# Performance work log

Measured on AMD Instinct MI355X. Metric: run time of the kernel, lower is better.

Reference implementation:

```python
import jax, jax.numpy as jnp
import numpy as np

TOP_K = 2

def setup_inputs() -> dict:
    key = jax.random.key(0)
    k1, k2 = jax.random.split(key)
    x = jax.random.normal(k1, (4, 4096, 4096), dtype=jnp.float32)
    # nn.Linear(hidden, experts, bias=False) weight: [num_experts, hidden]
    gate_w = jax.random.normal(k2, (64, 4096), dtype=jnp.float32) * (1.0 / np.sqrt(4096.0))
    return {"x": x, "gate_w": gate_w}

def reference(x, gate_w):
    # logits: [b, s, e] = x @ gate_w.T
    logits = jnp.einsum('bsh,eh->bse', x, gate_w)
    top_k_logits, top_k_indices = jax.lax.top_k(logits, TOP_K)  # [b, s, k]
    # softmax over top-k logits in float32, cast back to logits dtype
    probs = jax.nn.softmax(top_k_logits.astype(jnp.float32), axis=-1).astype(logits.dtype)
    return (logits, top_k_indices, probs)
```

## Files before the change

### kernel.cpp

```cpp
#include <hip/hip_runtime.h>
#include <math.h>

#define H 4096
#define E 64
#define BMROWS 16
#define NT 256
#define KQ 1024
#define BK 32
#define NWIN (KQ / BK)

typedef short bf16x8 __attribute__((ext_vector_type(8)));
typedef float f32x4  __attribute__((ext_vector_type(4)));

__device__ __forceinline__ unsigned f2bf_rne_u(float f) {
    unsigned u = __float_as_uint(f);
    return (u + 0x7fffu + ((u >> 16) & 1u)) >> 16;
}

__global__ __launch_bounds__(256) void convert_w(const float* __restrict__ w,
                                                 unsigned short* __restrict__ wh,
                                                 unsigned short* __restrict__ wl) {
    const int i = (blockIdx.x * 256 + threadIdx.x) * 4;
    float4 v = *(const float4*)(w + i);
    float vv[4] = {v.x, v.y, v.z, v.w};
    unsigned hh[4], ll[4];
#pragma unroll
    for (int j = 0; j < 4; ++j) {
        hh[j] = f2bf_rne_u(vv[j]);
        float r = vv[j] - __uint_as_float(hh[j] << 16);
        ll[j] = __float_as_uint(r) >> 16;
    }
    ushort4 h, l;
    h.x = (unsigned short)hh[0]; h.y = (unsigned short)hh[1];
    h.z = (unsigned short)hh[2]; h.w = (unsigned short)hh[3];
    l.x = (unsigned short)ll[0]; l.y = (unsigned short)ll[1];
    l.z = (unsigned short)ll[2]; l.w = (unsigned short)ll[3];
    *(ushort4*)(wh + i) = h;
    *(ushort4*)(wl + i) = l;
}

__device__ __forceinline__ void cvt8(const float4 a, const float4 b,
                                     bf16x8& hi, bf16x8& lo) {
    float v[8] = {a.x, a.y, a.z, a.w, b.x, b.y, b.z, b.w};
#pragma unroll
    for (int i = 0; i < 8; ++i) {
        const unsigned u = __float_as_uint(v[i]);
        const unsigned t = u + 0x7fffu + ((u >> 16) & 1u);
        const float    r = v[i] - __uint_as_float(t & 0xffff0000u);
        hi[i] = (short)(t >> 16);
        lo[i] = (short)(__float_as_uint(r) >> 16);
    }
}

__global__ __launch_bounds__(NT, 4) void router_kernel(
    const float* __restrict__ x,
    const unsigned short* __restrict__ wh,
    const unsigned short* __restrict__ wl,
    float* __restrict__ out, int M)
{
    __shared__ __align__(16) f32x4 merge[4][4][64];

    const int t    = threadIdx.x;
    const int lane = t & 63;
    const int wk   = t >> 6;
    const int m0   = blockIdx.x * BMROWS;
    const int col  = lane & 15;
    const int quad = lane >> 4;

    const int kbase = wk * KQ + quad * 8;

    const float* xp = x + (size_t)(m0 + col) * H + kbase;
    const unsigned short* whp = wh + (size_t)col * H + kbase;
    const unsigned short* wlp = wl + (size_t)col * H + kbase;

    f32x4 acc[4];
#pragma unroll
    for (int nt = 0; nt < 4; ++nt)
        acc[nt] = (f32x4){0.0f, 0.0f, 0.0f, 0.0f};

    float4 x0[2], x1[2], x2[2], x3[2];
    uint4  wr[8];

    auto loadx_into = [&](int win, float4 (&xb)[2]) {
        const int k = win * BK;
        xb[0] = *(const float4*)(xp + k);
        xb[1] = *(const float4*)(xp + k + 4);
    };
    auto loadw = [&](int win) {
        const int k = win * BK;
#pragma unroll
        for (int nt = 0; nt < 4; ++nt) {
            wr[nt]     = *(const uint4*)(whp + (size_t)(nt * 16) * H + k);
            wr[nt + 4] = *(const uint4*)(wlp + (size_t)(nt * 16) * H + k);
        }
    };

    auto step = [&](int win, float4 (&xc)[2], float4 (&xpref)[2]) {
        loadw(win);
        if (win + 3 < NWIN) loadx_into(win + 3, xpref);
        bf16x8 ah, al;
        cvt8(xc[0], xc[1], ah, al);
#pragma unroll
        for (int nt = 0; nt < 4; ++nt) {
            const bf16x8 bh = __builtin_bit_cast(bf16x8, wr[nt]);
            const bf16x8 bl = __builtin_bit_cast(bf16x8, wr[nt + 4]);
            acc[nt] = __builtin_amdgcn_mfma_f32_16x16x32_bf16(ah, bh, acc[nt], 0, 0, 0);
            acc[nt] = __builtin_amdgcn_mfma_f32_16x16x32_bf16(ah, bl, acc[nt], 0, 0, 0);
            acc[nt] = __builtin_amdgcn_mfma_f32_16x16x32_bf16(al, bh, acc[nt], 0, 0, 0);
        }
    };

    loadx_into(0, x0);
    loadx_into(1, x1);
    loadx_into(2, x2);

#pragma unroll 1
    for (int win = 0; win < NWIN; win += 4) {
        step(win,     x0, x3);
        step(win + 1, x1, x0);
        step(win + 2, x2, x1);
        step(win + 3, x3, x2);
    }

#pragma unroll
    for (int nt = 0; nt < 4; ++nt)
        merge[nt][wk][lane] = acc[nt];
    __syncthreads();

    if (wk != 0) return;

    f32x4 a2[4];
#pragma unroll
    for (int nt = 0; nt < 4; ++nt) {
        f32x4 s = acc[nt];
#pragma unroll
        for (int w = 1; w < 4; ++w)
            s += merge[nt][w][lane];
        a2[nt] = s;
    }

    float* logits   = out;
    float* idx_out  = out + (size_t)M * E;
    float* prob_out = idx_out + (size_t)M * 2;

    const int mrow = m0 + quad * 4;
#pragma unroll
    for (int r = 0; r < 4; ++r) {
#pragma unroll
        for (int nt = 0; nt < 4; ++nt)
            logits[(size_t)(mrow + r) * E + nt * 16 + col] = a2[nt][r];

        float v1 = a2[0][r], v2 = -INFINITY;
        int   i1 = col,      i2 = 0x7fffffff;
#pragma unroll
        for (int nt = 1; nt < 4; ++nt) {
            const float v = a2[nt][r];
            const int   e = nt * 16 + col;
            if (v > v1)      { v2 = v1; i2 = i1; v1 = v; i1 = e; }
            else if (v > v2) { v2 = v;  i2 = e; }
        }
#pragma unroll
        for (int mask = 1; mask < 16; mask <<= 1) {
            const float ov1 = __shfl_xor(v1, mask);
            const float ov2 = __shfl_xor(v2, mask);
            const int   oi1 = __shfl_xor(i1, mask);
            const int   oi2 = __shfl_xor(i2, mask);
            const bool afirst = (v1 > ov1) || (v1 == ov1 && i1 < oi1);
            float nv1, nv2; int ni1, ni2;
            if (afirst) {
                nv1 = v1; ni1 = i1;
                const bool s = (v2 > ov1) || (v2 == ov1 && i2 < oi1);
                nv2 = s ? v2 : ov1; ni2 = s ? i2 : oi1;
            } else {
                nv1 = ov1; ni1 = oi1;
                const bool s = (ov2 > v1) || (ov2 == v1 && oi2 < i1);
                nv2 = s ? ov2 : v1; ni2 = s ? oi2 : i1;
            }
            v1 = nv1; v2 = nv2; i1 = ni1; i2 = ni2;
        }
        if (col == 0) {
            const int m = mrow + r;
            const float e2 = __expf(v2 - v1);
            const float d  = 1.0f + e2;
            *(float2*)(idx_out  + (size_t)m * 2) = make_float2((float)i1, (float)i2);
            *(float2*)(prob_out + (size_t)m * 2) = make_float2(1.0f / d, e2 / d);
        }
    }
}

extern "C" void kernel_launch(void* const* d_in, const int* in_sizes, int n_in,
                              void* d_out, int out_size, void* d_ws, size_t ws_size,
                              hipStream_t stream) {
    const float* x = (const float*)d_in[0];
    const float* w = (const float*)d_in[1];
    unsigned short* wh = (unsigned short*)d_ws;
    unsigned short* wl = wh + (size_t)E * H;
    const int M = in_sizes[0] / H;

    hipLaunchKernelGGL(convert_w, dim3((E * H) / 1024), dim3(256), 0, stream,
                       w, wh, wl);
    hipLaunchKernelGGL(router_kernel, dim3(M / BMROWS), dim3(NT), 0, stream,
                       x, wh, wl, (float*)d_out, M);
}
```

Baseline: 453.4 us.

## Stage x tiles through LDS with async global_load_lds and double-buffer weights

Replaces the per-lane strided float4 loads of x with row-coalesced global_load_lds transfers into a 4-deep swizzled LDS ring per wave. Each wave then reads its MFMA operand layout back from LDS. Weight loads are double-buffered in registers, and explicit vmcnt waits with sched barriers pipeline memory against MFMA. The aim is better coalescing of x reads and more memory-level parallelism, at the cost of hand-tuned wait counts that could be fragile.

```diff
diff --git a/kernel.cpp b/kernel.cpp
--- a/kernel.cpp
+++ b/kernel.cpp
@@ -12,6 +12,9 @@
 typedef short bf16x8 __attribute__((ext_vector_type(8)));
 typedef float f32x4  __attribute__((ext_vector_type(4)));
 
+#define GLBP(p) ((const __attribute__((address_space(1))) void*)(p))
+#define LDSP(p) ((__attribute__((address_space(3))) void*)(p))
+
 __device__ __forceinline__ unsigned f2bf_rne_u(float f) {
     unsigned u = __float_as_uint(f);
     return (u + 0x7fffu + ((u >> 16) & 1u)) >> 16;
@@ -39,9 +42,9 @@
     *(ushort4*)(wl + i) = l;
 }
 
-__device__ __forceinline__ void cvt8(const float4 a, const float4 b,
+__device__ __forceinline__ void cvt8(const f32x4 a, const f32x4 b,
                                      bf16x8& hi, bf16x8& lo) {
-    float v[8] = {a.x, a.y, a.z, a.w, b.x, b.y, b.z, b.w};
+    float v[8] = {a[0], a[1], a[2], a[3], b[0], b[1], b[2], b[3]};
 #pragma unroll
     for (int i = 0; i < 8; ++i) {
         const unsigned u = __float_as_uint(v[i]);
@@ -58,7 +61,7 @@
     const unsigned short* __restrict__ wl,
     float* __restrict__ out, int M)
 {
-    __shared__ __align__(16) f32x4 merge[4][4][64];
+    __shared__ __align__(16) float smem[4 * 4 * 512];
 
     const int t    = threadIdx.x;
     const int lane = t & 63;
@@ -67,39 +70,45 @@
     const int col  = lane & 15;
     const int quad = lane >> 4;
 
-    const int kbase = wk * KQ + quad * 8;
-
-    const float* xp = x + (size_t)(m0 + col) * H + kbase;
-    const unsigned short* whp = wh + (size_t)col * H + kbase;
-    const unsigned short* wlp = wl + (size_t)col * H + kbase;
+    const int srow = lane >> 3;
+    const int scg  = (lane & 7) ^ srow;
+    const float* gx = x + (size_t)(m0 + srow) * H + wk * KQ + scg * 4;
+
+    const int r7  = col & 7;
+    const int sl0 = col * 8 + ((2 * quad    ) ^ r7);
+    const int sl1 = col * 8 + ((2 * quad + 1) ^ r7);
+
+    const unsigned short* whp = wh + (size_t)col * H + wk * KQ + quad * 8;
+    const unsigned short* wlp = wl + (size_t)col * H + wk * KQ + quad * 8;
 
     f32x4 acc[4];
 #pragma unroll
     for (int nt = 0; nt < 4; ++nt)
         acc[nt] = (f32x4){0.0f, 0.0f, 0.0f, 0.0f};
 
-    float4 x0[2], x1[2], x2[2], x3[2];
-    uint4  wr[8];
-
-    auto loadx_into = [&](int win, float4 (&xb)[2]) {
-        const int k = win * BK;
-        xb[0] = *(const float4*)(xp + k);
-        xb[1] = *(const float4*)(xp + k + 4);
+    uint4 wrA[8], wrB[8];
+
+    auto stage = [&](int win) {
+        float* l = smem + ((win & 3) * 4 + wk) * 512;
+        const float* g = gx + (size_t)win * BK;
+#pragma unroll
+        for (int j = 0; j < 2; ++j)
+            __builtin_amdgcn_global_load_lds(GLBP(g + (size_t)j * 8 * H),
+                                             LDSP(l + j * 256), 16, 0, 0);
     };
-    auto loadw = [&](int win) {
-        const int k = win * BK;
+    auto loadw = [&](int win, uint4 (&wr)[8]) {
+        const size_t k = (size_t)win * BK;
 #pragma unroll
         for (int nt = 0; nt < 4; ++nt) {
-            wr[nt]     = *(const uint4*)(whp + (size_t)(nt * 16) * H + k);
-            wr[nt + 4] = *(const uint4*)(wlp + (size_t)(nt * 16) * H + k);
+            wr[nt]     = *(const uint4*)(whp + (size_t)nt * 16 * H + k);
+            wr[nt + 4] = *(const uint4*)(wlp + (size_t)nt * 16 * H + k);
         }
     };
-
-    auto step = [&](int win, float4 (&xc)[2], float4 (&xpref)[2]) {
-        loadw(win);
-        if (win + 3 < NWIN) loadx_into(win + 3, xpref);
+    auto compute = [&](int win, const uint4 (&wr)[8]) {
+        const f32x4* sv = (const f32x4*)smem + (size_t)((win & 3) * 4 + wk) * 128;
+        const f32x4 c0 = sv[sl0], c1 = sv[sl1];
         bf16x8 ah, al;
-        cvt8(xc[0], xc[1], ah, al);
+        cvt8(c0, c1, ah, al);
 #pragma unroll
         for (int nt = 0; nt < 4; ++nt) {
             const bf16x8 bh = __builtin_bit_cast(bf16x8, wr[nt]);
@@ -110,21 +119,38 @@
         }
     };
 
-    loadx_into(0, x0);
-    loadx_into(1, x1);
-    loadx_into(2, x2);
+    stage(0);
+    stage(1);
+    stage(2);
+    __builtin_amdgcn_sched_barrier(0);
+    loadw(0, wrA);
 
 #pragma unroll 1
-    for (int win = 0; win < NWIN; win += 4) {
-        step(win,     x0, x3);
-        step(win + 1, x1, x0);
-        step(win + 2, x2, x1);
-        step(win + 3, x3, x2);
-    }
-
+    for (int k = 0; k < NWIN - 2; k += 2) {
+        loadw(k + 1, wrB);
+        stage(k + 3);
+        asm volatile("s_waitcnt vmcnt(22)" ::: "memory");
+        __builtin_amdgcn_sched_barrier(0);
+        compute(k, wrA);
+        loadw(k + 2, wrA);
+        if (k + 4 < NWIN) stage(k + 4);
+        asm volatile("s_waitcnt vmcnt(22)" ::: "memory");
+        __builtin_amdgcn_sched_barrier(0);
+        compute(k + 1, wrB);
+    }
+    loadw(31, wrB);
+    asm volatile("s_waitcnt vmcnt(22)" ::: "memory");
+    __builtin_amdgcn_sched_barrier(0);
+    compute(30, wrA);
+    asm volatile("s_waitcnt vmcnt(8)" ::: "memory");
+    __builtin_amdgcn_sched_barrier(0);
+    compute(31, wrB);
+
+    __syncthreads();
+    f32x4* mg = (f32x4*)smem;
 #pragma unroll
     for (int nt = 0; nt < 4; ++nt)
-        merge[nt][wk][lane] = acc[nt];
+        mg[(size_t)nt * 256 + wk * 64 + lane] = acc[nt];
     __syncthreads();
 
     if (wk != 0) return;
@@ -135,7 +161,7 @@
         f32x4 s = acc[nt];
 #pragma unroll
         for (int w = 1; w < 4; ++w)
-            s += merge[nt][w][lane];
+            s += mg[(size_t)nt * 256 + w * 64 + lane];
         a2[nt] = s;
     }
 
```

New measurement: 485.2 us. +7.0%, slower.
